# Performance work log

Measured on AMD Instinct MI355X. Metric: run time of the kernel, lower is better.

Reference implementation:

```python
import jax, jax.numpy as jnp
import numpy as np

H, KVH, D, HID = 32, 32, 128, 4096
THETA = 10000.0
EPS = 1e-5


def setup_inputs() -> dict:
    key = jax.random.key(0)
    ks = jax.random.split(key, 7)
    T = 2048
    return {
        "positions": jnp.arange(T, dtype=jnp.int32),
        "hidden_states": jax.random.normal(ks[0], (T, HID), dtype=jnp.float32),
        "w_qkv": jax.random.normal(ks[1], ((H + 2 * KVH) * D, HID), dtype=jnp.float32) * 0.02,
        "w_o": jax.random.normal(ks[2], (HID, H * D), dtype=jnp.float32) * 0.02,
        "q_norm_w": jax.random.uniform(ks[3], (H, D), dtype=jnp.float32),
        "q_norm_b": jax.random.normal(ks[4], (H, D), dtype=jnp.float32) * 0.02,
        "k_norm_w": jax.random.uniform(ks[5], (KVH, D), dtype=jnp.float32),
        "k_norm_b": jax.random.normal(ks[6], (KVH, D), dtype=jnp.float32) * 0.02,
    }


def _per_head_ln(x, w, b):
    # x: [T, H, D]; layer_norm over last dim without affine, then *w + b (per head)
    mu = jnp.mean(x, axis=-1, keepdims=True)
    var = jnp.mean(jnp.square(x - mu), axis=-1, keepdims=True)
    xn = (x - mu) * jax.lax.rsqrt(var + EPS)
    return xn * w + b


def _rope(x, positions):
    # neox-style rotate-half RoPE; x: [T, H, D]
    half = D // 2
    inv_freq = 1.0 / (THETA ** (jnp.arange(0, D, 2, dtype=jnp.float32) / D))  # [D/2]
    freqs = positions.astype(jnp.float32)[:, None] * inv_freq  # [T, D/2]
    cos = jnp.cos(freqs)[:, None, :]  # [T, 1, D/2]
    sin = jnp.sin(freqs)[:, None, :]
    x1, x2 = x[..., :half], x[..., half:]
    return jnp.concatenate([x1 * cos - x2 * sin, x2 * cos + x1 * sin], axis=-1)


def reference(positions, hidden_states, w_qkv, w_o, q_norm_w, q_norm_b, k_norm_w, k_norm_b):
    T = hidden_states.shape[0]
    qkv = hidden_states @ w_qkv.T  # [T, (H+2*KVH)*D]
    q, k, v = jnp.split(qkv, [H * D, (H + KVH) * D], axis=-1)
    q = q.reshape(T, H, D)
    k = k.reshape(T, KVH, D)
    v = v.reshape(T, KVH, D)
    q = _per_head_ln(q, q_norm_w, q_norm_b)
    k = _per_head_ln(k, k_norm_w, k_norm_b)
    q = _rope(q, positions)
    k = _rope(k, positions)
    scale = D ** -0.5
    scores = jnp.einsum("qhd,khd->hqk", q, k) * scale  # [H, T, T]
    causal = jnp.tril(jnp.ones((T, T), dtype=bool))
    scores = jnp.where(causal, scores, jnp.finfo(scores.dtype).min)
    probs = jax.nn.softmax(scores, axis=-1)
    attn = jnp.einsum("hqk,khd->qhd", probs, v).reshape(T, H * D)
    return attn @ w_o.T  # [T, HID]
```

## Files before the change

kernel.cpp:

```cpp
#include <hip/hip_runtime.h>
#include <cstdint>

typedef unsigned short u16;
typedef __attribute__((ext_vector_type(8))) __bf16 bf16x8;
typedef __attribute__((ext_vector_type(4))) float f32x4;

__device__ __forceinline__ u16 f2bf(float f) {
  unsigned int u = __builtin_bit_cast(unsigned int, f);
  unsigned int r = (u + 0x7fffu + ((u >> 16) & 1u)) >> 16;
  return (u16)r;
}
__device__ __forceinline__ float bf2f(u16 u) {
  return __builtin_bit_cast(float, (unsigned int)u << 16);
}

__device__ __forceinline__ void gload16(const u16* g, u16* l) {
  __builtin_amdgcn_global_load_lds((const __attribute__((address_space(1))) void*)g,
                                   (__attribute__((address_space(3))) void*)l, 16, 0, 0);
}

__device__ __forceinline__ int swz64i(int row, int col) {
  return row * 64 + (((col & 0x38) ^ ((row & 7) << 3)) | (col & 7));
}
__device__ __forceinline__ int swz128i(int row, int col) {
  return row * 128 + (((col & 0x78) ^ ((row & 7) << 3)) | (col & 7));
}

__global__ __launch_bounds__(256) void cvt_bf16_kernel(const float* __restrict__ in,
                                                       u16* __restrict__ out, long n4) {
  long i = (long)blockIdx.x * 256 + threadIdx.x;
  long stride = (long)gridDim.x * 256;
  const float4* in4 = (const float4*)in;
  uint2* out2 = (uint2*)out;
  for (long k = i; k < n4; k += stride) {
    float4 v = in4[k];
    uint2 o;
    o.x = (unsigned int)f2bf(v.x) | ((unsigned int)f2bf(v.y) << 16);
    o.y = (unsigned int)f2bf(v.z) | ((unsigned int)f2bf(v.w) << 16);
    out2[k] = o;
  }
}

__global__ __launch_bounds__(512, 2) void gemm192(const u16* __restrict__ A,
                                                  const u16* __restrict__ B,
                                                  u16* __restrict__ C,
                                                  int Ndim, int Kdim) {
  extern __shared__ __align__(16) u16 lds[];
  const int tid = threadIdx.x;
  const int lane = tid & 63, wave = tid >> 6;
  const int wr = wave >> 2, wc = wave & 3;
  const int l15 = lane & 15, l4 = lane >> 4;
  const int gx = gridDim.x;
  int lin = blockIdx.y * gx + blockIdx.x;
  const int xcd = lin & 7, ii = lin >> 3;
  const int bx = xcd * (gx >> 3) + (ii >> 3), by = ii & 7;
  const long arow = (long)by * 256, brow = (long)bx * 192;
  const int NT = Kdim >> 6;

  const int rowt = tid >> 3;
  const int koff = ((tid & 7) ^ (rowt & 7)) * 8;
  const u16* gA[4];
  const u16* gB[3];
  #pragma unroll
  for (int r = 0; r < 4; ++r) gA[r] = A + (size_t)(arow + rowt + r * 64) * Kdim + koff;
  #pragma unroll
  for (int r = 0; r < 3; ++r) gB[r] = B + (size_t)(brow + rowt + r * 64) * Kdim + koff;
  u16* const ldsB = lds + 49152;

  auto STA = [&](int u) {
    u16* d = lds + (u % 3) * 16384 + tid * 8;
    #pragma unroll
    for (int r = 0; r < 4; ++r) gload16(gA[r] + (size_t)u * 64, d + r * 4096);
  };
  auto STB = [&](int u) {
    u16* d = ldsB + (u & 1) * 12288 + tid * 8;
    #pragma unroll
    for (int r = 0; r < 3; ++r) gload16(gB[r] + (size_t)u * 64, d + r * 4096);
  };

  bf16x8 af[4][2], bfr[3][2];
  f32x4 acc[8][3] = {};
  int cks[2];
  #pragma unroll
  for (int kc = 0; kc < 2; ++kc) cks[kc] = (((kc * 4 + l4) ^ (l15 & 7)) * 8);

  auto LDA4 = [&](int u, int mh) {
    const u16* base = lds + (u % 3) * 16384 + (wr * 128 + mh * 64 + l15) * 64;
    #pragma unroll
    for (int m = 0; m < 4; ++m)
      #pragma unroll
      for (int kc = 0; kc < 2; ++kc)
        af[m][kc] = *(const bf16x8*)(base + m * 1024 + cks[kc]);
  };
  auto LDBall = [&](int u) {
    const u16* base = ldsB + (u & 1) * 12288 + (wc * 48 + l15) * 64;
    #pragma unroll
    for (int nh = 0; nh < 3; ++nh)
      #pragma unroll
      for (int kc = 0; kc < 2; ++kc)
        bfr[nh][kc] = *(const bf16x8*)(base + nh * 1024 + cks[kc]);
  };
  auto MM24 = [&](int mh) {
    #pragma unroll
    for (int kc = 0; kc < 2; ++kc)
      #pragma unroll
      for (int m = 0; m < 4; ++m)
        #pragma unroll
        for (int nh = 0; nh < 3; ++nh)
          acc[mh * 4 + m][nh] = __builtin_amdgcn_mfma_f32_16x16x32_bf16(
              af[m][kc], bfr[nh][kc], acc[mh * 4 + m][nh], 0, 0, 0);
  };

#define PH_BEGIN() do { __builtin_amdgcn_s_barrier();                         \
    asm volatile("s_waitcnt lgkmcnt(0)" ::: "memory");                        \
    __builtin_amdgcn_sched_barrier(0);                                        \
    __builtin_amdgcn_s_setprio(1); } while (0)
#define PH_END() do { __builtin_amdgcn_s_setprio(0);                          \
    __builtin_amdgcn_s_barrier(); } while (0)

  STA(0); STB(0); STA(1);
  asm volatile("s_waitcnt vmcnt(4)" ::: "memory");
  __builtin_amdgcn_s_barrier();

  for (int u = 0; u < NT; ++u) {
    LDA4(u, 0); LDBall(u);
    if (u + 1 < NT) STB(u + 1);
    PH_BEGIN(); MM24(0); PH_END();
    LDA4(u, 1);
    if (u + 2 < NT) STA(u + 2);
    PH_BEGIN(); MM24(1);
    __builtin_amdgcn_s_setprio(0);
    if (u + 2 < NT) { asm volatile("s_waitcnt vmcnt(4)" ::: "memory"); }
    else            { asm volatile("s_waitcnt vmcnt(0)" ::: "memory"); }
    __builtin_amdgcn_s_barrier();
  }
#undef PH_BEGIN
#undef PH_END

  #pragma unroll
  for (int m = 0; m < 8; ++m)
    #pragma unroll
    for (int nh = 0; nh < 3; ++nh)
      #pragma unroll
      for (int j = 0; j < 4; ++j) {
        long r = arow + wr * 128 + m * 16 + l4 * 4 + j;
        long c = brow + wc * 48 + nh * 16 + l15;
        C[r * Ndim + c] = f2bf(acc[m][nh][j]);
      }
}

__global__ __launch_bounds__(512, 2) void gemm256(const u16* __restrict__ A,
                                                  const u16* __restrict__ B,
                                                  float* __restrict__ C,
                                                  int Ndim, int Kdim) {
  extern __shared__ __align__(16) u16 lds[];
  const int tid = threadIdx.x;
  const int lane = tid & 63, wave = tid >> 6;
  const int wr = wave >> 2, wc = wave & 3;
  const int l15 = lane & 15, l4 = lane >> 4;
  const int gx = gridDim.x;
  int lin = blockIdx.y * gx + blockIdx.x;
  const int xcd = lin & 7, ii = lin >> 3;
  const int bx = xcd * (gx >> 3) + (ii >> 3), by = ii & 7;
  const long arow = (long)by * 256, brow = (long)bx * 128;
  const int NT = Kdim >> 6;

  const int rowt = tid >> 3;
  const int koff = ((tid & 7) ^ (rowt & 7)) * 8;
  const u16* gA[4];
  const u16* gB[2];
  #pragma unroll
  for (int r = 0; r < 4; ++r) gA[r] = A + (size_t)(arow + rowt + r * 64) * Kdim + koff;
  #pragma unroll
  for (int r = 0; r < 2; ++r) gB[r] = B + (size_t)(brow + rowt + r * 64) * Kdim + koff;

  auto STA = [&](int u) {
    u16* d = lds + (u % 3) * 16384 + tid * 8;
    #pragma unroll
    for (int r = 0; r < 4; ++r) gload16(gA[r] + (size_t)u * 64, d + r * 4096);
  };
  auto STB = [&](int u) {
    u16* d = lds + 49152 + (u & 1) * 8192 + tid * 8;
    #pragma unroll
    for (int r = 0; r < 2; ++r) gload16(gB[r] + (size_t)u * 64, d + r * 4096);
  };

  bf16x8 af[4][2], bfr[2][2];
  f32x4 acc[8][2] = {};
  int cks[2];
  #pragma unroll
  for (int kc = 0; kc < 2; ++kc) cks[kc] = (((kc * 4 + l4) ^ (l15 & 7)) * 8);

  auto LDA = [&](int u, int mh) {
    const u16* base = lds + (u % 3) * 16384 + (wr * 128 + mh * 64 + l15) * 64;
    #pragma unroll
    for (int m = 0; m < 4; ++m)
      #pragma unroll
      for (int kc = 0; kc < 2; ++kc)
        af[m][kc] = *(const bf16x8*)(base + m * 1024 + cks[kc]);
  };
  auto LDB = [&](int u) {
    const u16* base = lds + 49152 + (u & 1) * 8192 + (wc * 32 + l15) * 64;
    #pragma unroll
    for (int n = 0; n < 2; ++n)
      #pragma unroll
      for (int kc = 0; kc < 2; ++kc)
        bfr[n][kc] = *(const bf16x8*)(base + n * 1024 + cks[kc]);
  };
  auto MM = [&](int mh) {
    #pragma unroll
    for (int kc = 0; kc < 2; ++kc)
      #pragma unroll
      for (int m = 0; m < 4; ++m)
        #pragma unroll
        for (int n = 0; n < 2; ++n)
          acc[mh * 4 + m][n] =
            __builtin_amdgcn_mfma_f32_16x16x32_bf16(af[m][kc], bfr[n][kc],
                                                    acc[mh * 4 + m][n], 0, 0, 0);
  };

#define PH_BEGIN() do { __builtin_amdgcn_s_barrier();                         \
    asm volatile("s_waitcnt lgkmcnt(0)" ::: "memory");                        \
    __builtin_amdgcn_sched_barrier(0);                                        \
    __builtin_amdgcn_s_setprio(1); } while (0)

  STA(0); STB(0); STA(1); STB(1);
  asm volatile("s_waitcnt vmcnt(6)" ::: "memory");
  __builtin_amdgcn_s_barrier();

  for (int u = 0; u < NT; ++u) {
    LDA(u, 0); LDB(u);
    if (u + 2 < NT) STA(u + 2);
    PH_BEGIN(); MM(0);
    __builtin_amdgcn_s_setprio(0);
    __builtin_amdgcn_s_barrier();
    LDA(u, 1);
    if (u + 2 < NT) STB(u + 2);
    PH_BEGIN(); MM(1);
    __builtin_amdgcn_s_setprio(0);
    if (u + 2 < NT) { asm volatile("s_waitcnt vmcnt(6)" ::: "memory"); }
    else if (u + 1 < NT) { asm volatile("s_waitcnt vmcnt(0)" ::: "memory"); }
    __builtin_amdgcn_s_barrier();
  }
#undef PH_BEGIN

  #pragma unroll
  for (int M = 0; M < 8; ++M)
    #pragma unroll
    for (int n = 0; n < 2; ++n)
      #pragma unroll
      for (int j = 0; j < 4; ++j) {
        long r = arow + wr * 128 + M * 16 + l4 * 4 + j;
        long c = brow + wc * 32 + n * 16 + l15;
        C[r * Ndim + c] = acc[M][n][j];
      }
}

__global__ __launch_bounds__(256) void ln_rope_kernel(
    const u16* __restrict__ qkv, const int* __restrict__ pos,
    const float* __restrict__ qw, const float* __restrict__ qb2,
    const float* __restrict__ kw, const float* __restrict__ kb2,
    u16* __restrict__ qo, u16* __restrict__ ko, u16* __restrict__ vo, int T) {
  const int hh = blockIdx.x;
  const int t0 = blockIdx.y * 16 + (threadIdx.x >> 6) * 4;
  const int lane = threadIdx.x & 63;
  if (hh >= 64) {
    #pragma unroll
    for (int i = 0; i < 4; ++i) {
      int t = t0 + i;
      const u16* src = qkv + (size_t)t * 12288 + hh * 128;
      u16* dst = vo + ((size_t)(hh - 64) * T + t) * 128;
      dst[lane] = src[lane];
      dst[lane + 64] = src[lane + 64];
    }
    return;
  }
  bool isq = hh < 32;
  int hl = isq ? hh : hh - 32;
  const float* wp = (isq ? qw : kw) + hl * 128;
  const float* bp = (isq ? qb2 : kb2) + hl * 128;
  float w1 = wp[lane], w2 = wp[lane + 64];
  float b1 = bp[lane], b2 = bp[lane + 64];
  float invf = exp2f((float)lane * (-13.287712379549449f / 64.0f));
  u16* obase = (isq ? qo : ko) + (size_t)hl * T * 128;
  const float sc = isq ? 0.08838834764831845f : 1.0f;
  #pragma unroll
  for (int i = 0; i < 4; ++i) {
    int t = t0 + i;
    const u16* src = qkv + (size_t)t * 12288 + hh * 128;
    float x1 = bf2f(src[lane]), x2 = bf2f(src[lane + 64]);
    float s = x1 + x2;
    #pragma unroll
    for (int off = 32; off; off >>= 1) s += __shfl_xor(s, off);
    float mu = s * (1.0f / 128.0f);
    float d1 = x1 - mu, d2 = x2 - mu;
    float vs = d1 * d1 + d2 * d2;
    #pragma unroll
    for (int off = 32; off; off >>= 1) vs += __shfl_xor(vs, off);
    float rstd = rsqrtf(vs * (1.0f / 128.0f) + 1e-5f);
    float y1 = d1 * rstd * w1 + b1;
    float y2 = d2 * rstd * w2 + b2;
    float fr = (float)pos[t] * invf;
    float sn, cs;
    __sincosf(fr, &sn, &cs);
    float o1 = (y1 * cs - y2 * sn) * sc;
    float o2 = (y2 * cs + y1 * sn) * sc;
    u16* dst = obase + (size_t)t * 128;
    dst[lane] = f2bf(o1); dst[lane + 64] = f2bf(o2);
  }
}

__global__ __launch_bounds__(512, 2) void flash_kernel(
    const u16* __restrict__ qb, const u16* __restrict__ kb,
    const u16* __restrict__ vb, u16* __restrict__ attn, int T,
    const float* __restrict__ wo, u16* __restrict__ wo_bf) {
  extern __shared__ __align__(16) u16 flds[];
  const int tid = threadIdx.x;
  const int bid = blockIdx.x;
  if (bid >= 512) {
    const long n4 = (long)4096 * 4096 / 4;
    long i = (long)(bid - 512) * 512 + tid;
    const long stride = 256 * 512;
    const float4* in4 = (const float4*)wo;
    uint2* out2 = (uint2*)wo_bf;
    for (long k = i; k < n4; k += stride) {
      float4 v = in4[k];
      uint2 o;
      o.x = (unsigned int)f2bf(v.x) | ((unsigned int)f2bf(v.y) << 16);
      o.y = (unsigned int)f2bf(v.z) | ((unsigned int)f2bf(v.w) << 16);
      out2[k] = o;
    }
    return;
  }
  u16* const Ks = flds;
  u16* const Vt = flds + 8192;
  u16* const Ps = flds + 16384;
  const int lane = tid & 63, wave = tid >> 6;
  const int l15 = lane & 15, l4 = lane >> 4;
  const int nqt = T >> 7;
  const int h = bid & 31;
  const int qt = (bid < 256) ? (nqt - 1 - (bid >> 5)) : ((bid - 256) >> 5);
  const int qbase = qt * 128;
  const u16* Q  = qb + (size_t)h * T * 128;
  const u16* Kp = kb + (size_t)h * T * 128;
  const u16* Vp = vb + (size_t)h * T * 128;
  const int rK = tid >> 4, d8k = (tid & 15) * 8;
  const int rv = tid & 63, dv0 = (tid >> 6) * 8;
  u16* const Pw = Ps + wave * 1024;

  const int r0g = qbase + wave * 16;
  bf16x8 qf[4];
  #pragma unroll
  for (int kc = 0; kc < 4; ++kc)
    qf[kc] = *(const bf16x8*)&Q[(size_t)(r0g + l15) * 128 + kc * 32 + l4 * 8];

  float m_st[4], l_st[4];
  f32x4 o[8] = {};
  #pragma unroll
  for (int j = 0; j < 4; ++j) { m_st[j] = -1e30f; l_st[j] = 0.0f; }

  const int ntile = 2 * qt + 2;
  uint4 kr[2], vr[2];
  #pragma unroll
  for (int c = 0; c < 2; ++c) {
    kr[c] = *(const uint4*)&Kp[(size_t)(rK + 32 * c) * 128 + d8k];
    vr[c] = *(const uint4*)&Vp[(size_t)rv * 128 + dv0 + 64 * c];
  }
  for (int kt = 0; kt < ntile; ++kt) {
    const int kbase = kt * 64;
    #pragma unroll
    for (int c = 0; c < 2; ++c) {
      *(uint4*)&Ks[swz128i(rK + 32 * c, d8k)] = kr[c];
      const u16* pv = (const u16*)&vr[c];
      #pragma unroll
      for (int j = 0; j < 8; ++j) Vt[swz64i(dv0 + 64 * c + j, rv)] = pv[j];
    }
    __syncthreads();
    if (kt + 1 < ntile) {
      const int nb = kbase + 64;
      #pragma unroll
      for (int c = 0; c < 2; ++c) {
        kr[c] = *(const uint4*)&Kp[(size_t)(nb + rK + 32 * c) * 128 + d8k];
        vr[c] = *(const uint4*)&Vp[(size_t)(nb + rv) * 128 + dv0 + 64 * c];
      }
    }
    if (kbase <= r0g + 15) {
      f32x4 s[4] = {};
      __builtin_amdgcn_s_setprio(1);
      #pragma unroll
      for (int kc = 0; kc < 4; ++kc)
        #pragma unroll
        for (int nj = 0; nj < 4; ++nj) {
          bf16x8 kf = *(const bf16x8*)&Ks[swz128i(nj * 16 + l15, kc * 32 + l4 * 8)];
          s[nj] = __builtin_amdgcn_mfma_f32_16x16x32_bf16(qf[kc], kf, s[nj], 0, 0, 0);
        }
      __builtin_amdgcn_s_setprio(0);
      if (kbase + 63 > r0g) {
        #pragma unroll
        for (int nj = 0; nj < 4; ++nj)
          #pragma unroll
          for (int j = 0; j < 4; ++j) {
            int r = r0g + l4 * 4 + j;
            int cc = kbase + nj * 16 + l15;
            if (cc > r) s[nj][j] = -1e30f;
          }
      }
      float vmax[4];
      float dmax = -1e30f;
      #pragma unroll
      for (int j = 0; j < 4; ++j) {
        float v = fmaxf(fmaxf(s[0][j], s[1][j]), fmaxf(s[2][j], s[3][j]));
        #pragma unroll
        for (int off = 1; off < 16; off <<= 1) v = fmaxf(v, __shfl_xor(v, off));
        vmax[j] = v;
        dmax = fmaxf(dmax, v - m_st[j]);
      }
      if (!__all(dmax <= 8.0f)) {
        #pragma unroll
        for (int j = 0; j < 4; ++j) {
          float mn = fmaxf(m_st[j], vmax[j]);
          float scl = __expf(m_st[j] - mn);
          m_st[j] = mn;
          l_st[j] *= scl;
          #pragma unroll
          for (int nf = 0; nf < 8; ++nf) o[nf][j] *= scl;
        }
      }
      float sum[4] = {0.f, 0.f, 0.f, 0.f};
      #pragma unroll
      for (int nj = 0; nj < 4; ++nj)
        #pragma unroll
        for (int j = 0; j < 4; ++j) {
          float p = __expf(s[nj][j] - m_st[j]);
          s[nj][j] = p;
          sum[j] += p;
        }
      #pragma unroll
      for (int j = 0; j < 4; ++j) {
        #pragma unroll
        for (int off = 1; off < 16; off <<= 1) sum[j] += __shfl_xor(sum[j], off);
        l_st[j] += sum[j];
      }
      #pragma unroll
      for (int nj = 0; nj < 4; ++nj)
        #pragma unroll
        for (int j = 0; j < 4; ++j)
          Pw[swz64i(l4 * 4 + j, nj * 16 + l15)] = f2bf(s[nj][j]);
      asm volatile("s_waitcnt lgkmcnt(0)" ::: "memory");
      __builtin_amdgcn_sched_barrier(0);
      __builtin_amdgcn_s_setprio(1);
      #pragma unroll
      for (int kc = 0; kc < 2; ++kc) {
        bf16x8 pf = *(const bf16x8*)&Pw[swz64i(l15, kc * 32 + l4 * 8)];
        #pragma unroll
        for (int nf = 0; nf < 8; ++nf) {
          bf16x8 vf = *(const bf16x8*)&Vt[swz64i(nf * 16 + l15, kc * 32 + l4 * 8)];
          o[nf] = __builtin_amdgcn_mfma_f32_16x16x32_bf16(pf, vf, o[nf], 0, 0, 0);
        }
      }
      __builtin_amdgcn_s_setprio(0);
    }
    __syncthreads();
  }
  float rl[4];
  #pragma unroll
  for (int j = 0; j < 4; ++j) rl[j] = 1.0f / l_st[j];
  #pragma unroll
  for (int nf = 0; nf < 8; ++nf)
    #pragma unroll
    for (int j = 0; j < 4; ++j) {
      int r = r0g + l4 * 4 + j;
      int cc = h * 128 + nf * 16 + l15;
      attn[(size_t)r * 4096 + cc] = f2bf(o[nf][j] * rl[j]);
    }
}

extern "C" void kernel_launch(void* const* d_in, const int* in_sizes, int n_in,
                              void* d_out, int out_size, void* d_ws, size_t ws_size,
                              hipStream_t stream) {
  const int* positions = (const int*)d_in[0];
  const float* hidden  = (const float*)d_in[1];
  const float* w_qkv   = (const float*)d_in[2];
  const float* w_o     = (const float*)d_in[3];
  const float* qnw     = (const float*)d_in[4];
  const float* qnb     = (const float*)d_in[5];
  const float* knw     = (const float*)d_in[6];
  const float* knb     = (const float*)d_in[7];
  float* out = (float*)d_out;

  const int T = in_sizes[0];
  const int HID = 4096, NQKV = 12288, H = 32;

  char* ws = (char*)d_ws;
  u16* hid_bf  = (u16*)ws;
  u16* wreg    = (u16*)(ws + (size_t)T * HID * 2);
  u16* qkv_bf  = (u16*)(ws + (size_t)T * HID * 2 + (size_t)NQKV * HID * 2);

  u16* q_bf  = wreg;
  u16* k_bf  = q_bf + (size_t)H * T * 128;
  u16* v_bf  = k_bf + (size_t)H * T * 128;
  u16* at_bf = v_bf + (size_t)H * T * 128;
  u16* wo_bf = at_bf + (size_t)T * 4096;

  hipFuncSetAttribute(reinterpret_cast<const void*>(&gemm192),
                      hipFuncAttributeMaxDynamicSharedMemorySize, 147456);
  hipFuncSetAttribute(reinterpret_cast<const void*>(&gemm256),
                      hipFuncAttributeMaxDynamicSharedMemorySize, 131072);
  hipFuncSetAttribute(reinterpret_cast<const void*>(&flash_kernel),
                      hipFuncAttributeMaxDynamicSharedMemorySize, 49152);

  cvt_bf16_kernel<<<2048, 256, 0, stream>>>(hidden, hid_bf, (long)T * HID / 4);
  cvt_bf16_kernel<<<4096, 256, 0, stream>>>(w_qkv, wreg, (long)NQKV * HID / 4);
  gemm192<<<dim3(NQKV / 192, T / 256), 512, 147456, stream>>>(hid_bf, wreg, qkv_bf, NQKV, HID);
  ln_rope_kernel<<<dim3(96, T / 16), 256, 0, stream>>>(qkv_bf, positions, qnw, qnb, knw, knb,
                                                       q_bf, k_bf, v_bf, T);
  flash_kernel<<<768, 512, 49152, stream>>>(q_bf, k_bf, v_bf, at_bf, T, w_o, wo_bf);
  gemm256<<<dim3(HID / 128, T / 256), 512, 131072, stream>>>(at_bf, wo_bf, out, HID, HID);
}
```

Before: 475.7 us.

## Fuse fp32-to-bf16 weight conversion into the QKV GEMM loader

Removes the separate conversion kernel for w_qkv. The QKV GEMM now loads fp32 weight tiles into registers two K-steps ahead, converts them to bf16 and writes them into swizzled LDS, with vmcnt waits retuned for the new load mix. The K loop is unrolled by two so it can ping-pong between two register banks. This avoids writing and re-reading a bf16 copy of the weights, at the cost of reading fp32 weights once per row-block tile and of extra VGPR pressure that could cause spills or lower occupancy.

After: 505.3 us. 1.06x slower.

```diff
diff --git a/kernel.cpp b/kernel.cpp
--- a/kernel.cpp
+++ b/kernel.cpp
@@ -12,6 +12,12 @@
 }
 __device__ __forceinline__ float bf2f(u16 u) {
   return __builtin_bit_cast(float, (unsigned int)u << 16);
+}
+__device__ __forceinline__ bf16x8 pack8(float4 a, float4 b) {
+  bf16x8 r;
+  r[0] = (__bf16)a.x; r[1] = (__bf16)a.y; r[2] = (__bf16)a.z; r[3] = (__bf16)a.w;
+  r[4] = (__bf16)b.x; r[5] = (__bf16)b.y; r[6] = (__bf16)b.z; r[7] = (__bf16)b.w;
+  return r;
 }
 
 __device__ __forceinline__ void gload16(const u16* g, u16* l) {
@@ -42,7 +48,7 @@
 }
 
 __global__ __launch_bounds__(512, 2) void gemm192(const u16* __restrict__ A,
-                                                  const u16* __restrict__ B,
+                                                  const float* __restrict__ W,
                                                   u16* __restrict__ C,
                                                   int Ndim, int Kdim) {
   extern __shared__ __align__(16) u16 lds[];
@@ -60,11 +66,11 @@
   const int rowt = tid >> 3;
   const int koff = ((tid & 7) ^ (rowt & 7)) * 8;
   const u16* gA[4];
-  const u16* gB[3];
+  const float* gW[3];
   #pragma unroll
   for (int r = 0; r < 4; ++r) gA[r] = A + (size_t)(arow + rowt + r * 64) * Kdim + koff;
   #pragma unroll
-  for (int r = 0; r < 3; ++r) gB[r] = B + (size_t)(brow + rowt + r * 64) * Kdim + koff;
+  for (int r = 0; r < 3; ++r) gW[r] = W + (size_t)(brow + rowt + r * 64) * Kdim + koff;
   u16* const ldsB = lds + 49152;
 
   auto STA = [&](int u) {
@@ -72,10 +78,19 @@
     #pragma unroll
     for (int r = 0; r < 4; ++r) gload16(gA[r] + (size_t)u * 64, d + r * 4096);
   };
-  auto STB = [&](int u) {
+  float4 br0[3][2], br1[3][2];
+  auto GLB = [&](int u, float4 (*bank)[2]) {
+    #pragma unroll
+    for (int r = 0; r < 3; ++r) {
+      bank[r][0] = *(const float4*)(gW[r] + (size_t)u * 64);
+      bank[r][1] = *(const float4*)(gW[r] + (size_t)u * 64 + 4);
+    }
+  };
+  auto CVW = [&](int u, const float4 (*bank)[2]) {
     u16* d = ldsB + (u & 1) * 12288 + tid * 8;
     #pragma unroll
-    for (int r = 0; r < 3; ++r) gload16(gB[r] + (size_t)u * 64, d + r * 4096);
+    for (int r = 0; r < 3; ++r)
+      *(bf16x8*)(d + r * 4096) = pack8(bank[r][0], bank[r][1]);
   };
 
   bf16x8 af[4][2], bfr[3][2];
@@ -118,21 +133,31 @@
 #define PH_END() do { __builtin_amdgcn_s_setprio(0);                          \
     __builtin_amdgcn_s_barrier(); } while (0)
 
-  STA(0); STB(0); STA(1);
-  asm volatile("s_waitcnt vmcnt(4)" ::: "memory");
+  GLB(0, br0);
+  STA(0); STA(1);
+  asm volatile("s_waitcnt vmcnt(8)" ::: "memory");
+  CVW(0, br0);
+  GLB(1, br1);
+  asm volatile("s_waitcnt vmcnt(10)" ::: "memory");
+  asm volatile("s_waitcnt lgkmcnt(0)" ::: "memory");
   __builtin_amdgcn_s_barrier();
 
-  for (int u = 0; u < NT; ++u) {
+  auto TILE = [&](int u, float4 (*gbank)[2], const float4 (*cbank)[2]) {
     LDA4(u, 0); LDBall(u);
-    if (u + 1 < NT) STB(u + 1);
+    if (u + 2 < NT) { GLB(u + 2, gbank); STA(u + 2); }
     PH_BEGIN(); MM24(0); PH_END();
     LDA4(u, 1);
-    if (u + 2 < NT) STA(u + 2);
+    if (u + 2 < NT) { asm volatile("s_waitcnt vmcnt(10)" ::: "memory"); }
+    else            { asm volatile("s_waitcnt vmcnt(0)" ::: "memory"); }
+    if (u + 1 < NT) CVW(u + 1, cbank);
     PH_BEGIN(); MM24(1);
     __builtin_amdgcn_s_setprio(0);
-    if (u + 2 < NT) { asm volatile("s_waitcnt vmcnt(4)" ::: "memory"); }
-    else            { asm volatile("s_waitcnt vmcnt(0)" ::: "memory"); }
     __builtin_amdgcn_s_barrier();
+  };
+
+  for (int u = 0; u < NT; u += 2) {
+    TILE(u, br0, br1);
+    TILE(u + 1, br1, br0);
   }
 #undef PH_BEGIN
 #undef PH_END
@@ -510,8 +535,7 @@
                       hipFuncAttributeMaxDynamicSharedMemorySize, 49152);
 
   cvt_bf16_kernel<<<2048, 256, 0, stream>>>(hidden, hid_bf, (long)T * HID / 4);
-  cvt_bf16_kernel<<<4096, 256, 0, stream>>>(w_qkv, wreg, (long)NQKV * HID / 4);
-  gemm192<<<dim3(NQKV / 192, T / 256), 512, 147456, stream>>>(hid_bf, wreg, qkv_bf, NQKV, HID);
+  gemm192<<<dim3(NQKV / 192, T / 256), 512, 147456, stream>>>(hid_bf, w_qkv, qkv_bf, NQKV, HID);
   ln_rope_kernel<<<dim3(96, T / 16), 256, 0, stream>>>(qkv_bf, positions, qnw, qnb, knw, knb,
                                                        q_bf, k_bf, v_bf, T);
   flash_kernel<<<768, 512, 49152, stream>>>(q_bf, k_bf, v_bf, at_bf, T, w_o, wo_bf);
```
